# Optimization experiments

Hardware: AMD Instinct MI355X
Metric: run time of the kernel (lower is better)

## Reference

```python
import jax, jax.numpy as jnp
import numpy as np

B = 64            # batch
C = 23            # chromosomes
E = 1024          # embedding_dim (eos)
D = 1024          # d_model
BOT = 128         # bottleneck_dim (embedding table width)
BINS = 8192       # bins per chromosome (num_bins_list entries)
NUM_BINS = C * BINS
S = 3             # num_states


def setup_inputs() -> dict:
    key = jax.random.key(0)
    ks = jax.random.split(key, 7)
    eos_emb = jax.random.normal(ks[0], (B, C, E), dtype=jnp.float32)
    # embedding table: indices used are 1..NUM_BINS (cum starts at 1), so NUM_BINS+2 rows
    emb_table = jax.random.normal(ks[1], (NUM_BINS + 2, BOT), dtype=jnp.float32) * 0.02
    Wb = jax.random.normal(ks[2], (D, BOT), dtype=jnp.float32) * 0.02   # bin_projection (no bias)
    We = jax.random.normal(ks[3], (D, E), dtype=jnp.float32) * 0.02     # eos_projection weight
    be = jax.random.normal(ks[4], (D,), dtype=jnp.float32) * 0.02       # eos_projection bias
    Wfc = jax.random.normal(ks[5], (S, 2 * D), dtype=jnp.float32) * 0.02  # fc weight
    bfc = jax.random.normal(ks[6], (S,), dtype=jnp.float32) * 0.02        # fc bias
    return {"eos_emb": eos_emb, "emb_table": emb_table, "Wb": Wb,
            "We": We, "be": be, "Wfc": Wfc, "bfc": bfc}


def reference(eos_emb, emb_table, Wb, We, be, Wfc, bfc):
    # eos_projection (use_eos_proj=True): [B, C, E] -> [B, C, D]
    eos = jnp.einsum('bce,de->bcd', eos_emb, We) + be
    # embedding lookup for all bins: indices 1..NUM_BINS (contiguous across chromosomes)
    idx = 1 + jnp.arange(NUM_BINS)
    # bin_projection (bottleneck_dim != d_model): [NUM_BINS, BOT] -> [NUM_BINS, D]
    bin_emb = jnp.einsum('nk,dk->nd', emb_table[idx], Wb).reshape(C, BINS, D)
    # fc on concat([bin_emb, eos]) == bin_emb @ W1^T + eos @ W2^T + b (avoids materializing concat)
    W1, W2 = Wfc[:, :D], Wfc[:, D:]
    part_bin = jnp.einsum('cnd,sd->cns', bin_emb, W1)   # [C, BINS, S]
    part_eos = jnp.einsum('bcd,sd->bcs', eos, W2)        # [B, C, S]
    # original returns list of 23 tensors [B, BINS, S]; stacked here as [B, C, BINS, S]
    out = jax.nn.relu(part_bin[None] + part_eos[:, :, None, :] + bfc)
    return out
```

## Files before the change

kernel.cpp:

```cpp
#include <hip/hip_runtime.h>

#define B_    64
#define C_    23
#define E_    1024
#define D_    1024
#define BOT_  128
#define BINS_ 8192
#define S_    3
#define NUMBINS (C_*BINS_)

typedef float f32x4 __attribute__((ext_vector_type(4)));

#define WS_M   0
#define WS_N   512
#define WS_C0  3584
#define WS_PE  3600

__global__ __launch_bounds__(256) void kprep(const float* __restrict__ Wb,
                                             const float* __restrict__ We,
                                             const float* __restrict__ be,
                                             const float* __restrict__ Wfc,
                                             const float* __restrict__ bfc,
                                             float* __restrict__ ws) {
    const int bx = blockIdx.x;
    const int t  = threadIdx.x;

    if (bx == 72) {
        int wave = t >> 6, lane = t & 63;
        if (wave < 3) {
            const float* w2 = Wfc + wave * 2 * D_ + D_;
            float acc = 0.f;
            #pragma unroll
            for (int j = 0; j < D_ / 64; j++) {
                int d = lane + j * 64;
                acc += w2[d] * be[d];
            }
            #pragma unroll
            for (int off = 32; off; off >>= 1) acc += __shfl_down(acc, off);
            if (lane == 0) ws[WS_C0 + wave] = acc + bfc[wave];
        }
        return;
    }

    __shared__ float wv[3072];
    __shared__ float red[256];

    const int og   = t & 15;
    const int dgrp = t >> 4;

    const float* src;
    int ostride, obase, wofs;
    float* dst0;
    int dstride;

    if (bx < 64) {
        int e0 = bx * 16;
        src = We; ostride = E_; obase = e0; wofs = D_;
        dst0 = ws + WS_N + e0; dstride = E_;
    } else {
        int k0 = (bx - 64) * 16;
        src = Wb; ostride = BOT_; obase = k0; wofs = 0;
        dst0 = ws + WS_M + k0; dstride = BOT_;
    }

    for (int i = t; i < 3072; i += 256) {
        int s = i >> 10, d = i & 1023;
        wv[i] = Wfc[s * 2 * D_ + wofs + d];
    }
    __syncthreads();

    const float* p  = src + (size_t)(dgrp * 64) * ostride + obase + og;
    const float* w0 = wv + dgrp * 64;
    float a0 = 0.f, a1 = 0.f, a2 = 0.f;
    #pragma unroll 8
    for (int i = 0; i < 64; i++) {
        float v = p[(size_t)i * ostride];
        a0 += w0[i] * v;
        a1 += w0[1024 + i] * v;
        a2 += w0[2048 + i] * v;
    }
    float accs[3] = {a0, a1, a2};
    for (int s = 0; s < 3; s++) {
        __syncthreads();
        red[t] = accs[s];
        #pragma unroll
        for (int off = 128; off >= 16; off >>= 1) {
            __syncthreads();
            if (t < off) red[t] += red[t + off];
        }
        if (t < 16) dst0[s * dstride + t] = red[t];
    }
}

__global__ __launch_bounds__(256) void kpe(const float* __restrict__ eos,
                                           float* ws) {
    int wave = threadIdx.x >> 6;
    int lane = threadIdx.x & 63;
    int row  = blockIdx.x * 4 + wave;
    const float* x  = eos + (size_t)row * E_;
    const float* N0 = ws + WS_N;
    float a0 = 0.f, a1 = 0.f, a2 = 0.f;
    #pragma unroll
    for (int j = 0; j < E_ / 64; j++) {
        int i = lane + j * 64;
        float v = x[i];
        a0 += v * N0[i];
        a1 += v * N0[1024 + i];
        a2 += v * N0[2048 + i];
    }
    #pragma unroll
    for (int off = 32; off; off >>= 1) {
        a0 += __shfl_down(a0, off);
        a1 += __shfl_down(a1, off);
        a2 += __shfl_down(a2, off);
    }
    if (lane == 0) {
        float* pe = ws + WS_PE + row * 3;
        pe[0] = a0 + ws[WS_C0 + 0];
        pe[1] = a1 + ws[WS_C0 + 1];
        pe[2] = a2 + ws[WS_C0 + 2];
    }
}

__global__ __launch_bounds__(256) void kmain(const float* __restrict__ table,
                                             const float* __restrict__ ws,
                                             float* __restrict__ out) {
    const int t  = threadIdx.x;
    const int c  = blockIdx.y;
    const int n0 = blockIdx.x * 256;

    const int w  = t >> 6;
    const int l  = t & 63;
    const int h  = l >> 5;
    const int kk = l & 31;

    __shared__ float P[64 * 97];
    __shared__ float pbl[192];
    __shared__ float pel[192];

    f32x4 M0 = ((const f32x4*)(ws + WS_M      ))[kk];
    f32x4 M1 = ((const f32x4*)(ws + WS_M + 128))[kk];
    f32x4 M2 = ((const f32x4*)(ws + WS_M + 256))[kk];

    if (t < 192) {
        int b = t / 3, s = t - b * 3;
        pel[t] = ws[WS_PE + (b * C_ + c) * 3 + s];
    }

    const float* base = table + (size_t)(1 + c * BINS_ + n0) * BOT_ + kk * 4;

    f32x4 va[8], vb[8];
    #pragma unroll
    for (int i = 0; i < 8; i++) {
        int rl = (w * 8 + i) * 2 + h;
        va[i] = *(const f32x4*)(base + (size_t)rl * BOT_);
    }

    #pragma unroll
    for (int bb = 0; bb < 4; bb++) {
        #pragma unroll
        for (int i = 0; i < 8; i++) {
            int rl = (w * 8 + i) * 2 + h;
            f32x4 v = (bb & 1) ? vb[i] : va[i];
            float* pp = &P[rl * 97 + kk * 3];
            pp[0] = v.x * M0.x + v.y * M0.y + v.z * M0.z + v.w * M0.w;
            pp[1] = v.x * M1.x + v.y * M1.y + v.z * M1.z + v.w * M1.w;
            pp[2] = v.x * M2.x + v.y * M2.y + v.z * M2.z + v.w * M2.w;
        }
        if (bb < 3) {
            #pragma unroll
            for (int i = 0; i < 8; i++) {
                int rl = (w * 8 + i) * 2 + h;
                f32x4 ld = *(const f32x4*)(base + (size_t)((bb + 1) * 64 + rl) * BOT_);
                if (bb & 1) va[i] = ld; else vb[i] = ld;
            }
        }
        __syncthreads();
        if (t < 192) {
            int s = t >> 6, ro = t & 63;
            const float* pr = &P[ro * 97 + s];
            float acc = 0.f;
            #pragma unroll
            for (int k = 0; k < 32; k++) acc += pr[k * 3];
            pbl[ro * 3 + s] = acc;
        }
        __syncthreads();
        {
            int b  = t / 48;
            int p4 = t - b * 48;
            const float* ob = out + ((size_t)c * BINS_ + n0 + bb * 64) * 3;
            #pragma unroll
            for (int j = 0; j < 12; j++) {
                f32x4 pv = *(const f32x4*)&pbl[p4 * 4];
                int s0 = p4 % 3;
                int s1 = (s0 + 1 == 3) ? 0 : s0 + 1;
                int s2 = (s1 + 1 == 3) ? 0 : s1 + 1;
                const float* pe = &pel[b * 3];
                f32x4 o;
                o.x = fmaxf(pv.x + pe[s0], 0.f);
                o.y = fmaxf(pv.y + pe[s1], 0.f);
                o.z = fmaxf(pv.z + pe[s2], 0.f);
                o.w = fmaxf(pv.w + pe[s0], 0.f);
                f32x4* dst = (f32x4*)(ob + (size_t)b * (C_ * BINS_ * 3)) + p4;
                __builtin_nontemporal_store(o, dst);
                b += 5; p4 += 16;
                if (p4 >= 48) { p4 -= 48; b += 1; }
            }
        }
    }
}

extern "C" void kernel_launch(void* const* d_in, const int* in_sizes, int n_in,
                              void* d_out, int out_size, void* d_ws, size_t ws_size,
                              hipStream_t stream) {
    const float* eos   = (const float*)d_in[0];
    const float* table = (const float*)d_in[1];
    const float* Wb    = (const float*)d_in[2];
    const float* We    = (const float*)d_in[3];
    const float* be    = (const float*)d_in[4];
    const float* Wfc   = (const float*)d_in[5];
    const float* bfc   = (const float*)d_in[6];
    float* out = (float*)d_out;
    float* ws  = (float*)d_ws;

    kprep<<<73, 256, 0, stream>>>(Wb, We, be, Wfc, bfc, ws);
    kpe<<<368, 256, 0, stream>>>(eos, ws);
    dim3 g(32, 23);
    kmain<<<g, 256, 0, stream>>>(table, ws, out);
}
```

Baseline: 51.66 us.

## Fuse eos projection into main kernel and swizzle blocks across XCDs

Removes the separate kpe launch and computes the per-(batch, chromosome) eos partial sums inside each kmain block using a shared-memory reduction. The grid becomes 1D and is remapped so blocks of the same chromosome land on the same XCD, improving L2 reuse of the eos slice. This trades one kernel launch and a ws round trip for redundant eos reads and FMAs in every block of a chromosome.

New measurement: 54.63 us. 1.06x slower.

```diff
diff --git a/kernel.cpp b/kernel.cpp
--- a/kernel.cpp
+++ b/kernel.cpp
@@ -14,7 +14,6 @@
 #define WS_M   0
 #define WS_N   512
 #define WS_C0  3584
-#define WS_PE  3600
 
 __global__ __launch_bounds__(256) void kprep(const float* __restrict__ Wb,
                                              const float* __restrict__ We,
@@ -92,42 +91,15 @@
     }
 }
 
-__global__ __launch_bounds__(256) void kpe(const float* __restrict__ eos,
-                                           float* ws) {
-    int wave = threadIdx.x >> 6;
-    int lane = threadIdx.x & 63;
-    int row  = blockIdx.x * 4 + wave;
-    const float* x  = eos + (size_t)row * E_;
-    const float* N0 = ws + WS_N;
-    float a0 = 0.f, a1 = 0.f, a2 = 0.f;
-    #pragma unroll
-    for (int j = 0; j < E_ / 64; j++) {
-        int i = lane + j * 64;
-        float v = x[i];
-        a0 += v * N0[i];
-        a1 += v * N0[1024 + i];
-        a2 += v * N0[2048 + i];
-    }
-    #pragma unroll
-    for (int off = 32; off; off >>= 1) {
-        a0 += __shfl_down(a0, off);
-        a1 += __shfl_down(a1, off);
-        a2 += __shfl_down(a2, off);
-    }
-    if (lane == 0) {
-        float* pe = ws + WS_PE + row * 3;
-        pe[0] = a0 + ws[WS_C0 + 0];
-        pe[1] = a1 + ws[WS_C0 + 1];
-        pe[2] = a2 + ws[WS_C0 + 2];
-    }
-}
-
 __global__ __launch_bounds__(256) void kmain(const float* __restrict__ table,
+                                             const float* __restrict__ eos,
                                              const float* __restrict__ ws,
                                              float* __restrict__ out) {
     const int t  = threadIdx.x;
-    const int c  = blockIdx.y;
-    const int n0 = blockIdx.x * 256;
+    const int d_  = blockIdx.x;
+    const int g   = (d_ & 7) * 92 + (d_ >> 3);
+    const int c   = g >> 5;
+    const int n0  = (g & 31) * 256;
 
     const int w  = t >> 6;
     const int l  = t & 63;
@@ -141,11 +113,6 @@
     f32x4 M0 = ((const f32x4*)(ws + WS_M      ))[kk];
     f32x4 M1 = ((const f32x4*)(ws + WS_M + 128))[kk];
     f32x4 M2 = ((const f32x4*)(ws + WS_M + 256))[kk];
-
-    if (t < 192) {
-        int b = t / 3, s = t - b * 3;
-        pel[t] = ws[WS_PE + (b * C_ + c) * 3 + s];
-    }
 
     const float* base = table + (size_t)(1 + c * BINS_ + n0) * BOT_ + kk * 4;
 
@@ -155,6 +122,51 @@
         int rl = (w * 8 + i) * 2 + h;
         va[i] = *(const f32x4*)(base + (size_t)rl * BOT_);
     }
+
+    {
+        const f32x4* Nq = (const f32x4*)(ws + WS_N);
+        f32x4 nq[12];
+        #pragma unroll
+        for (int s = 0; s < 3; s++)
+            #pragma unroll
+            for (int j = 0; j < 4; j++)
+                nq[s * 4 + j] = Nq[s * 256 + l + 64 * j];
+        const f32x4* eq = (const f32x4*)eos;
+        #pragma unroll
+        for (int rr = 0; rr < 16; rr++) {
+            int r = w * 16 + rr;
+            size_t eb = ((size_t)r * C_ + c) * 256;
+            f32x4 e0 = eq[eb + l];
+            f32x4 e1 = eq[eb + l + 64];
+            f32x4 e2 = eq[eb + l + 128];
+            f32x4 e3 = eq[eb + l + 192];
+            float p0, p1, p2;
+            #pragma unroll
+            for (int s = 0; s < 3; s++) {
+                f32x4 a = nq[s * 4], b4 = nq[s * 4 + 1], c4 = nq[s * 4 + 2], d4 = nq[s * 4 + 3];
+                float ps = e0.x * a.x + e0.y * a.y + e0.z * a.z + e0.w * a.w
+                         + e1.x * b4.x + e1.y * b4.y + e1.z * b4.z + e1.w * b4.w
+                         + e2.x * c4.x + e2.y * c4.y + e2.z * c4.z + e2.w * c4.w
+                         + e3.x * d4.x + e3.y * d4.y + e3.z * d4.z + e3.w * d4.w;
+                ps += __shfl_xor(ps, 32);
+                if (s == 0) p0 = ps; else if (s == 1) p1 = ps; else p2 = ps;
+            }
+            if (h == 0) {
+                float* pp = &P[r * 97 + kk * 3];
+                pp[0] = p0; pp[1] = p1; pp[2] = p2;
+            }
+        }
+    }
+    __syncthreads();
+    if (t < 192) {
+        int s = t >> 6, ro = t & 63;
+        const float* pr = &P[ro * 97 + s];
+        float acc = 0.f;
+        #pragma unroll
+        for (int k = 0; k < 32; k++) acc += pr[k * 3];
+        pel[ro * 3 + s] = acc + ws[WS_C0 + s];
+    }
+    __syncthreads();
 
     #pragma unroll
     for (int bb = 0; bb < 4; bb++) {
@@ -224,7 +236,5 @@
     float* ws  = (float*)d_ws;
 
     kprep<<<73, 256, 0, stream>>>(Wb, We, be, Wfc, bfc, ws);
-    kpe<<<368, 256, 0, stream>>>(eos, ws);
-    dim3 g(32, 23);
-    kmain<<<g, 256, 0, stream>>>(table, ws, out);
+    kmain<<<736, 256, 0, stream>>>(table, eos, ws, out);
 }
```

## Give each wave its own row strip to remove block-wide barriers in kmain

Applied to the files above, without the earlier changes.

kmain now assigns each wave a contiguous 64-row strip and handles it in four 16-row chunks, each staged in a per-wave shared buffer. The two __syncthreads per 64-row step go away, replaced by wave-local reductions and stores of 16 rows × 3 states. Partial products are written as padded f32x4 to reduce bank conflicts. In exchange each store burst covers only 48 floats per batch row instead of 192, which shortens contiguous write segments. Correctness also now depends on lockstep wave execution between the shared-memory write and the read.

Result: slower. 56.09 us (+8.6%).

```diff
diff --git a/kernel.cpp b/kernel.cpp
--- a/kernel.cpp
+++ b/kernel.cpp
@@ -134,64 +134,66 @@
     const int h  = l >> 5;
     const int kk = l & 31;
 
-    __shared__ float P[64 * 97];
-    __shared__ float pbl[192];
+    __shared__ f32x4 P4[4][16 * 33];
+    __shared__ float pbw[4][192];
     __shared__ float pel[192];
+
+    if (t < 192) {
+        int b = t / 3, s = t - b * 3;
+        pel[t] = ws[WS_PE + (b * C_ + c) * 3 + s];
+    }
+    __syncthreads();
 
     f32x4 M0 = ((const f32x4*)(ws + WS_M      ))[kk];
     f32x4 M1 = ((const f32x4*)(ws + WS_M + 128))[kk];
     f32x4 M2 = ((const f32x4*)(ws + WS_M + 256))[kk];
 
-    if (t < 192) {
-        int b = t / 3, s = t - b * 3;
-        pel[t] = ws[WS_PE + (b * C_ + c) * 3 + s];
-    }
-
-    const float* base = table + (size_t)(1 + c * BINS_ + n0) * BOT_ + kk * 4;
-
-    f32x4 va[8], vb[8];
-    #pragma unroll
-    for (int i = 0; i < 8; i++) {
-        int rl = (w * 8 + i) * 2 + h;
-        va[i] = *(const f32x4*)(base + (size_t)rl * BOT_);
-    }
-
-    #pragma unroll
-    for (int bb = 0; bb < 4; bb++) {
+    const float* base = table + (size_t)(1 + c * BINS_ + n0 + w * 64) * BOT_ + kk * 4;
+    float* ob = out + ((size_t)c * BINS_ + n0 + w * 64) * 3;
+    f32x4* pstrip = P4[w];
+    float* pw = pbw[w];
+
+    f32x4 ra[8], rb[8];
+    #pragma unroll
+    for (int i = 0; i < 8; i++)
+        ra[i] = *(const f32x4*)(base + (size_t)(i * 2 + h) * BOT_);
+
+    #pragma unroll
+    for (int cc = 0; cc < 4; cc++) {
+        if (cc < 3) {
+            #pragma unroll
+            for (int i = 0; i < 8; i++) {
+                f32x4 ld = *(const f32x4*)(base + (size_t)((cc + 1) * 16 + i * 2 + h) * BOT_);
+                if (cc & 1) ra[i] = ld; else rb[i] = ld;
+            }
+        }
         #pragma unroll
         for (int i = 0; i < 8; i++) {
-            int rl = (w * 8 + i) * 2 + h;
-            f32x4 v = (bb & 1) ? vb[i] : va[i];
-            float* pp = &P[rl * 97 + kk * 3];
-            pp[0] = v.x * M0.x + v.y * M0.y + v.z * M0.z + v.w * M0.w;
-            pp[1] = v.x * M1.x + v.y * M1.y + v.z * M1.z + v.w * M1.w;
-            pp[2] = v.x * M2.x + v.y * M2.y + v.z * M2.z + v.w * M2.w;
-        }
-        if (bb < 3) {
-            #pragma unroll
-            for (int i = 0; i < 8; i++) {
-                int rl = (w * 8 + i) * 2 + h;
-                f32x4 ld = *(const f32x4*)(base + (size_t)((bb + 1) * 64 + rl) * BOT_);
-                if (bb & 1) va[i] = ld; else vb[i] = ld;
-            }
-        }
-        __syncthreads();
-        if (t < 192) {
-            int s = t >> 6, ro = t & 63;
-            const float* pr = &P[ro * 97 + s];
+            f32x4 v = (cc & 1) ? rb[i] : ra[i];
+            int rl = i * 2 + h;
+            f32x4 p;
+            p.x = v.x * M0.x + v.y * M0.y + v.z * M0.z + v.w * M0.w;
+            p.y = v.x * M1.x + v.y * M1.y + v.z * M1.z + v.w * M1.w;
+            p.z = v.x * M2.x + v.y * M2.y + v.z * M2.z + v.w * M2.w;
+            p.w = 0.f;
+            pstrip[rl * 33 + kk] = p;
+        }
+        if (l < 48) {
+            int ro = l / 3, s = l - ro * 3;
+            const float* pr = (const float*)&pstrip[ro * 33] + s;
             float acc = 0.f;
             #pragma unroll
-            for (int k = 0; k < 32; k++) acc += pr[k * 3];
-            pbl[ro * 3 + s] = acc;
-        }
-        __syncthreads();
+            for (int k = 0; k < 32; k++) acc += pr[k * 4];
+            pw[cc * 48 + l] = acc;
+        }
         {
-            int b  = t / 48;
-            int p4 = t - b * 48;
-            const float* ob = out + ((size_t)c * BINS_ + n0 + bb * 64) * 3;
+            int f  = l;
+            int b  = f / 12;
+            int dp = f - b * 12;
             #pragma unroll
             for (int j = 0; j < 12; j++) {
-                f32x4 pv = *(const f32x4*)&pbl[p4 * 4];
+                int p4 = cc * 12 + dp;
+                f32x4 pv = *(const f32x4*)&pw[p4 * 4];
                 int s0 = p4 % 3;
                 int s1 = (s0 + 1 == 3) ? 0 : s0 + 1;
                 int s2 = (s1 + 1 == 3) ? 0 : s1 + 1;
@@ -201,10 +203,9 @@
                 o.y = fmaxf(pv.y + pe[s1], 0.f);
                 o.z = fmaxf(pv.z + pe[s2], 0.f);
                 o.w = fmaxf(pv.w + pe[s0], 0.f);
-                f32x4* dst = (f32x4*)(ob + (size_t)b * (C_ * BINS_ * 3)) + p4;
-                __builtin_nontemporal_store(o, dst);
-                b += 5; p4 += 16;
-                if (p4 >= 48) { p4 -= 48; b += 1; }
+                __builtin_nontemporal_store(o, (f32x4*)(ob + (size_t)b * (C_ * BINS_ * 3)) + p4);
+                b += 5; dp += 4;
+                if (dp >= 12) { dp -= 12; b += 1; }
             }
         }
     }
```
